# Optimization experiments

Hardware: AMD Instinct MI355X
Metric: run time of the kernel (lower is better)

Reference implementation:

```python
import jax, jax.numpy as jnp
import numpy as np

B, S, D, H = 2, 2048, 256, 8


def setup_inputs() -> dict:
    key = jax.random.key(0)
    ks = jax.random.split(key, 9)
    s = 1.0 / np.sqrt(D)
    x = jax.random.normal(ks[0], (B, S, D), dtype=jnp.float32)
    Wq = jax.random.normal(ks[1], (H, D, D), dtype=jnp.float32) * s
    Wk = jax.random.normal(ks[2], (H, D, D), dtype=jnp.float32) * s
    Wv = jax.random.normal(ks[3], (H, D, D), dtype=jnp.float32) * s
    bq = jnp.zeros((H, D), dtype=jnp.float32)
    bk = jnp.zeros((H, D), dtype=jnp.float32)
    bv = jnp.zeros((H, D), dtype=jnp.float32)
    Wo = jax.random.normal(ks[4], (H * D, D), dtype=jnp.float32) * (1.0 / np.sqrt(H * D))
    bo = jnp.zeros((D,), dtype=jnp.float32)
    return {"x": x, "Wq": Wq, "bq": bq, "Wk": Wk, "bk": bk, "Wv": Wv, "bv": bv, "Wo": Wo, "bo": bo}


def reference(x, Wq, bq, Wk, bk, Wv, bv, Wo, bo):
    # Per-head Q/K/V projections, batched over heads via einsum.
    # q,k,v: [B, H, S, D]
    q = jnp.einsum('bsd,hde->bhse', x, Wq) + bq[None, :, None, :]
    k = jnp.einsum('bsd,hde->bhse', x, Wk) + bk[None, :, None, :]
    v = jnp.einsum('bsd,hde->bhse', x, Wv) + bv[None, :, None, :]
    scale = 1.0 / jnp.sqrt(jnp.asarray(D, dtype=x.dtype))
    scores = jnp.einsum('bhse,bhte->bhst', q, k) * scale  # [B,H,S,S]
    attn = jax.nn.softmax(scores, axis=-1)
    o = jnp.einsum('bhst,bhte->bhse', attn, v)  # [B,H,S,D]
    # Concat heads along feature dim: [B,S,H*D]
    concat = o.transpose(0, 2, 1, 3).reshape(B, S, H * D)
    return concat @ Wo + bo
```

## Files before the change

### kernel.cpp

```cpp
#include <hip/hip_runtime.h>

typedef __bf16 bf16x8 __attribute__((ext_vector_type(8)));
typedef __bf16 bf16x4 __attribute__((ext_vector_type(4)));
typedef float  f32x4  __attribute__((ext_vector_type(4)));
typedef float  f32x16 __attribute__((ext_vector_type(16)));

#define DEVI __device__ __forceinline__

DEVI bf16x8 ld8(const __bf16* p) { return *reinterpret_cast<const bf16x8*>(p); }
DEVI f32x4 mfma16(bf16x8 a, bf16x8 b, f32x4 c) {
  return __builtin_amdgcn_mfma_f32_16x16x32_bf16(a, b, c, 0, 0, 0);
}
DEVI f32x16 mfma32(bf16x8 a, bf16x8 b, f32x16 c) {
  return __builtin_amdgcn_mfma_f32_32x32x16_bf16(a, b, c, 0, 0, 0);
}
DEVI void gl_lds16(const void* g, void* l) {
  __builtin_amdgcn_global_load_lds((__attribute__((address_space(1))) void*)g,
                                   (__attribute__((address_space(3))) void*)l, 16, 0, 0);
}
DEVI unsigned pk2(float a, float b) {
  union { __bf16 h[2]; unsigned u; } x;
  x.h[0] = (__bf16)a; x.h[1] = (__bf16)b; return x.u;
}

#if __has_builtin(__builtin_amdgcn_exp2f)
#define EXP2(x) __builtin_amdgcn_exp2f(x)
#else
#define EXP2(x) exp2f(x)
#endif

__global__ __launch_bounds__(256) void k_prep(
    const float* __restrict__ x, const float* __restrict__ Wq,
    const float* __restrict__ Wk, const float* __restrict__ Wv,
    const float* __restrict__ Wo, __bf16* __restrict__ xb,
    __bf16* __restrict__ Wt, __bf16* __restrict__ Woh, __bf16* __restrict__ Wol) {
  const int bid = blockIdx.x;
  if (bid < 1024) {
    const int i = bid * 256 + threadIdx.x;
    f32x4 v = reinterpret_cast<const f32x4*>(x)[i];
    bf16x4 o;
    o[0] = (__bf16)v[0]; o[1] = (__bf16)v[1]; o[2] = (__bf16)v[2]; o[3] = (__bf16)v[3];
    reinterpret_cast<bf16x4*>(xb)[i] = o;
    return;
  }
  __shared__ float t[32][33];
  const int flat = bid - 1024;
  const float* in; __bf16* oh; __bf16* ol = nullptr;
  int R, C, c0, r0;
  bool lo = false;
  if (flat < 1536) {
    const int which = flat >> 9, rem = flat & 511;
    const int h = rem >> 6, tt = rem & 63;
    c0 = (tt & 7) * 32; r0 = (tt >> 3) * 32;
    const float* Wsrc = which == 0 ? Wq : which == 1 ? Wk : Wv;
    in = Wsrc + h * 65536;
    oh = Wt + which * 524288 + h * 65536;
    R = 256; C = 256;
  } else {
    const int rem = flat - 1536;
    c0 = (rem & 7) * 32; r0 = (rem >> 3) * 32;
    in = Wo; oh = Woh; ol = Wol; lo = true;
    R = 2048; C = 256;
  }
  const int tx = threadIdx.x & 31, ty = threadIdx.x >> 5;
  #pragma unroll
  for (int k = 0; k < 32; k += 8)
    t[ty + k][tx] = in[(size_t)(r0 + ty + k) * C + c0 + tx];
  __syncthreads();
  #pragma unroll
  for (int k = 0; k < 32; k += 8) {
    const float v = t[tx][ty + k];
    const size_t o = (size_t)(c0 + ty + k) * R + r0 + tx;
    const __bf16 h = (__bf16)v;
    oh[o] = h;
    if (lo) ol[o] = (__bf16)(v - (float)h);
  }
}

__global__ __launch_bounds__(256) void k_qkv(
    const __bf16* __restrict__ xb, const __bf16* __restrict__ Wt,
    const float* __restrict__ bq, const float* __restrict__ bk, const float* __restrict__ bv,
    __bf16* __restrict__ Qb, __bf16* __restrict__ Kb, __bf16* __restrict__ Vtb) {
  const int wl = threadIdx.x >> 6, lane = threadIdx.x & 63;
  const int g = lane >> 4, qc = lane & 15;
  const int which = blockIdx.z >> 3, h = blockIdx.z & 7;
  const int sblk = blockIdx.x * 256;
  const int s0 = sblk + wl * 64;
  const int e0 = blockIdx.y * 64;
  const __bf16* Wm = Wt + ((size_t)blockIdx.z << 16);
  const float* bias = (which == 0 ? bq : which == 1 ? bk : bv) + h * 256;
  const int b = sblk >> 11;
  const int bh = b * 8 + h;
  const int sm0 = s0 & 2047;
  f32x4 acc[4][4] = {};

  if (which == 2) {
    #pragma unroll
    for (int kk = 0; kk < 8; kk++) {
      bf16x8 af[4], bf[4];
      #pragma unroll
      for (int ai = 0; ai < 4; ai++)
        af[ai] = ld8(xb + (size_t)(s0 + ai * 16 + qc) * 256 + kk * 32 + g * 8);
      #pragma unroll
      for (int bj = 0; bj < 4; bj++)
        bf[bj] = ld8(Wm + (size_t)(e0 + bj * 16 + qc) * 256 + kk * 32 + g * 8);
      #pragma unroll
      for (int ai = 0; ai < 4; ai++)
        #pragma unroll
        for (int bj = 0; bj < 4; bj++)
          acc[ai][bj] = mfma16(af[ai], bf[bj], acc[ai][bj]);
    }
    #pragma unroll
    for (int bj = 0; bj < 4; bj++) {
      const int e = e0 + bj * 16 + qc;
      const float be = bias[e];
      #pragma unroll
      for (int ai = 0; ai < 4; ai++) {
        bf16x4 pk;
        #pragma unroll
        for (int r = 0; r < 4; r++) pk[r] = (__bf16)(acc[ai][bj][r] + be);
        *reinterpret_cast<bf16x4*>(Vtb + ((size_t)(bh * 256 + e)) * 2048 +
                                   sm0 + ai * 16 + g * 4) = pk;
      }
    }
  } else {
    #pragma unroll
    for (int kk = 0; kk < 8; kk++) {
      bf16x8 af[4], bf[4];
      #pragma unroll
      for (int ai = 0; ai < 4; ai++)
        af[ai] = ld8(Wm + (size_t)(e0 + ai * 16 + qc) * 256 + kk * 32 + g * 8);
      #pragma unroll
      for (int bj = 0; bj < 4; bj++)
        bf[bj] = ld8(xb + (size_t)(s0 + bj * 16 + qc) * 256 + kk * 32 + g * 8);
      #pragma unroll
      for (int ai = 0; ai < 4; ai++)
        #pragma unroll
        for (int bj = 0; bj < 4; bj++)
          acc[ai][bj] = mfma16(af[ai], bf[bj], acc[ai][bj]);
    }
    const float sc = (which == 0) ? 0.0625f * 1.4426950408889634f : 1.0f;
    __bf16* Out = (which == 0) ? Qb : Kb;
    float be[4][4];
    #pragma unroll
    for (int ai = 0; ai < 4; ai++)
      #pragma unroll
      for (int r = 0; r < 4; r++) be[ai][r] = bias[e0 + ai * 16 + g * 4 + r];
    #pragma unroll
    for (int ai = 0; ai < 4; ai++)
      #pragma unroll
      for (int bj = 0; bj < 4; bj++) {
        const int srow = sm0 + bj * 16 + qc;
        bf16x4 pk;
        #pragma unroll
        for (int r = 0; r < 4; r++)
          pk[r] = (__bf16)((acc[ai][bj][r] + be[ai][r]) * sc);
        *reinterpret_cast<bf16x4*>(Out + ((size_t)(bh * 2048 + srow)) * 256 +
                                   e0 + ai * 16 + g * 4) = pk;
      }
  }
}

__global__ __launch_bounds__(256) void k_attn(
    const __bf16* __restrict__ Qb, const __bf16* __restrict__ Kb,
    const __bf16* __restrict__ Vtb, __bf16* __restrict__ Oh, __bf16* __restrict__ Ol) {
  __shared__ __align__(16) unsigned char smem[131072];
  const int tid = threadIdx.x;
  const int wl = tid >> 6, lane = tid & 63;
  const int hi = lane >> 5, q = lane & 31;

  const int bid = blockIdx.x;
  const int s = (bid & 7) * 32 + (bid >> 3);
  const int bh = s >> 4, qt = s & 15;

  const int q0w = qt * 128 + wl * 32;
  const char* Kg = (const char*)Kb + ((size_t)bh * 2048) * 512;
  const char* Vg = (const char*)Vtb + (size_t)bh * 256 * 4096;
  const __bf16* Qp = Qb + ((size_t)(bh * 2048 + q0w + q)) * 256;

  bf16x8 qf[16];
  #pragma unroll
  for (int kk = 0; kk < 16; kk++) qf[kk] = ld8(Qp + kk * 16 + hi * 8);

  f32x16 acc[8];
  #pragma unroll
  for (int i = 0; i < 8; i++)
    #pragma unroll
    for (int e = 0; e < 16; e++) acc[i][e] = 0.f;

  auto stage = [&](int nb, int t) {
    unsigned char* kbp = smem + nb * 32768 + wl * 8192;
    unsigned char* vbp = smem + 65536 + nb * 32768 + wl * 8192;
    #pragma unroll
    for (int j = 0; j < 8; j++) {
      const int O = wl * 8192 + j * 1024 + lane * 16;
      const int kv = O >> 9;
      const int c = ((O >> 4) & 31) ^ (kv & 15);
      gl_lds16(Kg + (size_t)t * 32768 + (size_t)kv * 512 + c * 16, kbp + j * 1024);
    }
    #pragma unroll
    for (int j = 0; j < 8; j++) {
      const int O = wl * 8192 + j * 1024 + lane * 16;
      const int sb = O >> 10;
      const int kvh = (O >> 9) & 1;
      const int dlo = (O >> 6) & 7;
      const int ci = (O >> 4) & 3;
      const int d = sb * 8 + dlo;
      gl_lds16(Vg + (size_t)d * 4096 + (size_t)t * 128 + kvh * 64 + ((ci ^ (sb & 3)) << 4),
               vbp + j * 1024);
    }
  };

  float m_run = -3.0e38f, l_run = 0.f;
  stage(0, 0);
  __syncthreads();

  for (int t = 0; t < 32; t++) {
    const int cur = t & 1;
    const unsigned char* kbc = smem + cur * 32768;
    const unsigned char* vbc = smem + 65536 + cur * 32768;
    if (t < 31) stage(cur ^ 1, t + 1);

    f32x16 st0, st1;
    #pragma unroll
    for (int e = 0; e < 16; e++) { st0[e] = 0.f; st1[e] = 0.f; }
    __builtin_amdgcn_s_setprio(1);
    #pragma unroll
    for (int kk = 0; kk < 16; kk++) {
      const int o0 = q * 512 + ((((kk << 1) + hi) ^ (q & 15)) << 4);
      bf16x8 k0 = *reinterpret_cast<const bf16x8*>(kbc + o0);
      bf16x8 k1 = *reinterpret_cast<const bf16x8*>(kbc + o0 + 16384);
      st0 = mfma32(k0, qf[kk], st0);
      st1 = mfma32(k1, qf[kk], st1);
    }
    __builtin_amdgcn_s_setprio(0);

    f32x16 mx;
    #pragma unroll
    for (int r = 0; r < 16; r++) mx[r] = fmaxf(st0[r], st1[r]);
    #pragma unroll
    for (int w2 = 8; w2 > 0; w2 >>= 1)
      #pragma unroll
      for (int r = 0; r < w2; r++) mx[r] = fmaxf(mx[r], mx[r + w2]);
    const float rmax = fmaxf(mx[0], __shfl_xor(mx[0], 32));
    if (__any(rmax > m_run + 8.0f)) {
      const float m_new = fmaxf(rmax, m_run);
      const float alpha = EXP2(m_run - m_new);
      m_run = m_new;
      l_run *= alpha;
      #pragma unroll
      for (int r = 0; r < 16; r++) {
        const float ar = __shfl(alpha, (r & 3) + 8 * (r >> 2) + 4 * hi);
        #pragma unroll
        for (int dt = 0; dt < 8; dt++) acc[dt][r] *= ar;
      }
    }
    f32x16 sm_;
    #pragma unroll
    for (int r = 0; r < 16; r++) {
      st0[r] = EXP2(st0[r] - m_run);
      st1[r] = EXP2(st1[r] - m_run);
      sm_[r] = st0[r] + st1[r];
    }
    #pragma unroll
    for (int w2 = 8; w2 > 0; w2 >>= 1)
      #pragma unroll
      for (int r = 0; r < w2; r++) sm_[r] += sm_[r + w2];
    l_run += sm_[0] + __shfl_xor(sm_[0], 32);

    bf16x8 pa[4];
    #define MKCHUNK(STV, H2, OUT) {                          \
      const unsigned L0 = pk2(STV[H2 * 8 + 0], STV[H2 * 8 + 1]);  \
      const unsigned L1 = pk2(STV[H2 * 8 + 2], STV[H2 * 8 + 3]);  \
      const unsigned H0 = pk2(STV[H2 * 8 + 4], STV[H2 * 8 + 5]);  \
      const unsigned H1 = pk2(STV[H2 * 8 + 6], STV[H2 * 8 + 7]);  \
      const unsigned xL0 = __shfl_xor(L0, 32), xL1 = __shfl_xor(L1, 32); \
      const unsigned xH0 = __shfl_xor(H0, 32), xH1 = __shfl_xor(H1, 32); \
      unsigned pw[4];                                        \
      pw[0] = hi ? xH0 : L0;  pw[1] = hi ? xH1 : L1;         \
      pw[2] = hi ? H0 : xL0;  pw[3] = hi ? H1 : xL1;         \
      OUT = *reinterpret_cast<bf16x8*>(pw); }
    MKCHUNK(st0, 0, pa[0]); MKCHUNK(st0, 1, pa[1]);
    MKCHUNK(st1, 0, pa[2]); MKCHUNK(st1, 1, pa[3]);
    #undef MKCHUNK

    __builtin_amdgcn_s_setprio(1);
    #pragma unroll
    for (int dt = 0; dt < 8; dt++) {
      const int d = dt * 32 + q;
      const int base = (d >> 3) * 1024 + (d & 7) * 64;
      const int key = (d >> 3) & 3;
      #pragma unroll
      for (int c = 0; c < 4; c++) {
        const int off = base + (c >> 1) * 512 +
                        (((((c & 1) << 1) | hi) ^ key) << 4);
        bf16x8 vf = *reinterpret_cast<const bf16x8*>(vbc + off);
        acc[dt] = mfma32(pa[c], vf, acc[dt]);
      }
    }
    __builtin_amdgcn_s_setprio(0);
    __syncthreads();
  }

  float linv[16];
  #pragma unroll
  for (int r = 0; r < 16; r++)
    linv[r] = 1.f / __shfl(l_run, (r & 3) + 8 * (r >> 2) + 4 * hi);
  const int b = bh >> 3, h = bh & 7;
  #pragma unroll
  for (int dt = 0; dt < 8; dt++) {
    #pragma unroll
    for (int r = 0; r < 16; r++) {
      const float v = acc[dt][r] * linv[r];
      const int qrow = (r & 3) + 8 * (r >> 2) + 4 * hi;
      const size_t off = (size_t)b * (2048 * 2048) +
                         (size_t)(q0w + qrow) * 2048 + h * 256 + dt * 32 + q;
      const __bf16 hv = (__bf16)v;
      Oh[off] = hv;
      Ol[off] = (__bf16)(v - (float)hv);
    }
  }
}

__global__ __launch_bounds__(256) void k_out(
    const __bf16* __restrict__ Oh, const __bf16* __restrict__ Ol,
    const __bf16* __restrict__ Wh, const __bf16* __restrict__ Wl,
    const float* __restrict__ bo, float* __restrict__ out) {
  const int w = threadIdx.x >> 6, lane = threadIdx.x & 63;
  const int g = lane >> 4, qc = lane & 15;
  const int m0 = blockIdx.x * 64 + w * 16, n0 = blockIdx.y * 64;
  const int k0 = blockIdx.z * 1024;
  f32x4 acc[4] = {};
  const __bf16* ah_p = Oh + (size_t)(m0 + qc) * 2048 + k0 + g * 8;
  const __bf16* al_p = Ol + (size_t)(m0 + qc) * 2048 + k0 + g * 8;
  for (int kk = 0; kk < 32; kk++) {
    bf16x8 ah = ld8(ah_p + kk * 32);
    bf16x8 al = ld8(al_p + kk * 32);
    #pragma unroll
    for (int nt = 0; nt < 4; nt++) {
      const size_t nrow = (size_t)(n0 + nt * 16 + qc) * 2048 + k0 + kk * 32 + g * 8;
      bf16x8 bh = ld8(Wh + nrow);
      bf16x8 bl = ld8(Wl + nrow);
      acc[nt] = mfma16(ah, bh, acc[nt]);
      acc[nt] = mfma16(al, bh, acc[nt]);
      acc[nt] = mfma16(ah, bl, acc[nt]);
    }
  }
  #pragma unroll
  for (int nt = 0; nt < 4; nt++) {
    const int n = n0 + nt * 16 + qc;
    const float bb = (blockIdx.z == 0) ? bo[n] : 0.f;
    #pragma unroll
    for (int r = 0; r < 4; r++)
      unsafeAtomicAdd(&out[(m0 + g * 4 + r) * 256 + n], acc[nt][r] + bb);
  }
}

extern "C" void kernel_launch(void* const* d_in, const int* in_sizes, int n_in,
                              void* d_out, int out_size, void* d_ws, size_t ws_size,
                              hipStream_t stream) {
  const float* x  = (const float*)d_in[0];
  const float* Wq = (const float*)d_in[1];
  const float* bq = (const float*)d_in[2];
  const float* Wk = (const float*)d_in[3];
  const float* bk = (const float*)d_in[4];
  const float* Wv = (const float*)d_in[5];
  const float* bv = (const float*)d_in[6];
  const float* Wo = (const float*)d_in[7];
  const float* bo = (const float*)d_in[8];
  char* p = (char*)d_ws;
  __bf16* xb  = (__bf16*)(p);
  __bf16* Wt  = (__bf16*)(p + (2ull  << 20));
  __bf16* Woh = (__bf16*)(p + (5ull  << 20));
  __bf16* Wol = (__bf16*)(p + (6ull  << 20));
  __bf16* Qb  = (__bf16*)(p + (7ull  << 20));
  __bf16* Kb  = (__bf16*)(p + (23ull << 20));
  __bf16* Vtb = (__bf16*)(p + (39ull << 20));
  __bf16* Ohb = (__bf16*)(p + (55ull << 20));
  __bf16* Olb = (__bf16*)(p + (71ull << 20));

  k_prep<<<dim3(3072), dim3(256), 0, stream>>>(x, Wq, Wk, Wv, Wo, xb, Wt, Woh, Wol);
  k_qkv<<<dim3(16, 4, 24), dim3(256), 0, stream>>>(xb, Wt, bq, bk, bv, Qb, Kb, Vtb);
  k_attn<<<dim3(256), dim3(256), 0, stream>>>(Qb, Kb, Vtb, Ohb, Olb);
  (void)hipMemsetAsync(d_out, 0, (size_t)out_size * sizeof(float), stream);
  k_out<<<dim3(64, 4, 2), dim3(256), 0, stream>>>(Ohb, Olb, Woh, Wol, bo, (float*)d_out);
}
```

Measured before the change: 255.4 us.

## Fuse Q and K projections per block, drop setprio, deepen out-proj split-K

The QKV kernel now computes Q and K together in one block, sharing the x fragment loads across both weight matrices, and runs V in separate blocks, which cuts the grid from 24 to 16 z-slices. The s_setprio hints around the MFMA loops in the attention kernel are removed. The output projection's split-K factor goes from 2 to 4, halving each block's K range and doubling the number of atomic partial sums into the output. The QK fusion doubles accumulator registers per thread, which may lower occupancy.

```diff
diff --git a/kernel.cpp b/kernel.cpp
--- a/kernel.cpp
+++ b/kernel.cpp
@@ -83,18 +83,18 @@
     __bf16* __restrict__ Qb, __bf16* __restrict__ Kb, __bf16* __restrict__ Vtb) {
   const int wl = threadIdx.x >> 6, lane = threadIdx.x & 63;
   const int g = lane >> 4, qc = lane & 15;
-  const int which = blockIdx.z >> 3, h = blockIdx.z & 7;
+  const int h = blockIdx.z >> 1, isV = blockIdx.z & 1;
   const int sblk = blockIdx.x * 256;
   const int s0 = sblk + wl * 64;
   const int e0 = blockIdx.y * 64;
-  const __bf16* Wm = Wt + ((size_t)blockIdx.z << 16);
-  const float* bias = (which == 0 ? bq : which == 1 ? bk : bv) + h * 256;
   const int b = sblk >> 11;
   const int bh = b * 8 + h;
   const int sm0 = s0 & 2047;
-  f32x4 acc[4][4] = {};
-
-  if (which == 2) {
+
+  if (isV) {
+    const __bf16* Wm = Wt + 2 * 524288 + (size_t)h * 65536;
+    const float* bias = bv + h * 256;
+    f32x4 acc[4][4] = {};
     #pragma unroll
     for (int kk = 0; kk < 8; kk++) {
       bf16x8 af[4], bf[4];
@@ -124,40 +124,51 @@
       }
     }
   } else {
+    const __bf16* WmQ = Wt + (size_t)h * 65536;
+    const __bf16* WmK = Wt + 524288 + (size_t)h * 65536;
+    f32x4 accq[4][4] = {}, acck[4][4] = {};
     #pragma unroll
     for (int kk = 0; kk < 8; kk++) {
-      bf16x8 af[4], bf[4];
-      #pragma unroll
-      for (int ai = 0; ai < 4; ai++)
-        af[ai] = ld8(Wm + (size_t)(e0 + ai * 16 + qc) * 256 + kk * 32 + g * 8);
+      bf16x8 aq[4], ak[4], bf[4];
+      #pragma unroll
+      for (int ai = 0; ai < 4; ai++) {
+        aq[ai] = ld8(WmQ + (size_t)(e0 + ai * 16 + qc) * 256 + kk * 32 + g * 8);
+        ak[ai] = ld8(WmK + (size_t)(e0 + ai * 16 + qc) * 256 + kk * 32 + g * 8);
+      }
       #pragma unroll
       for (int bj = 0; bj < 4; bj++)
         bf[bj] = ld8(xb + (size_t)(s0 + bj * 16 + qc) * 256 + kk * 32 + g * 8);
       #pragma unroll
       for (int ai = 0; ai < 4; ai++)
         #pragma unroll
-        for (int bj = 0; bj < 4; bj++)
-          acc[ai][bj] = mfma16(af[ai], bf[bj], acc[ai][bj]);
-    }
-    const float sc = (which == 0) ? 0.0625f * 1.4426950408889634f : 1.0f;
-    __bf16* Out = (which == 0) ? Qb : Kb;
-    float be[4][4];
-    #pragma unroll
-    for (int ai = 0; ai < 4; ai++)
-      #pragma unroll
-      for (int r = 0; r < 4; r++) be[ai][r] = bias[e0 + ai * 16 + g * 4 + r];
-    #pragma unroll
-    for (int ai = 0; ai < 4; ai++)
+        for (int bj = 0; bj < 4; bj++) {
+          accq[ai][bj] = mfma16(aq[ai], bf[bj], accq[ai][bj]);
+          acck[ai][bj] = mfma16(ak[ai], bf[bj], acck[ai][bj]);
+        }
+    }
+    const float sc = 0.0625f * 1.4426950408889634f;
+    #pragma unroll
+    for (int ai = 0; ai < 4; ai++) {
+      float beq[4], bek[4];
+      #pragma unroll
+      for (int r = 0; r < 4; r++) {
+        beq[r] = bq[h * 256 + e0 + ai * 16 + g * 4 + r];
+        bek[r] = bk[h * 256 + e0 + ai * 16 + g * 4 + r];
+      }
       #pragma unroll
       for (int bj = 0; bj < 4; bj++) {
         const int srow = sm0 + bj * 16 + qc;
-        bf16x4 pk;
-        #pragma unroll
-        for (int r = 0; r < 4; r++)
-          pk[r] = (__bf16)((acc[ai][bj][r] + be[ai][r]) * sc);
-        *reinterpret_cast<bf16x4*>(Out + ((size_t)(bh * 2048 + srow)) * 256 +
-                                   e0 + ai * 16 + g * 4) = pk;
-      }
+        const size_t base = ((size_t)(bh * 2048 + srow)) * 256 + e0 + ai * 16 + g * 4;
+        bf16x4 pq, pk;
+        #pragma unroll
+        for (int r = 0; r < 4; r++) {
+          pq[r] = (__bf16)((accq[ai][bj][r] + beq[r]) * sc);
+          pk[r] = (__bf16)(acck[ai][bj][r] + bek[r]);
+        }
+        *reinterpret_cast<bf16x4*>(Qb + base) = pq;
+        *reinterpret_cast<bf16x4*>(Kb + base) = pk;
+      }
+    }
   }
 }
 
@@ -224,7 +235,6 @@
     f32x16 st0, st1;
     #pragma unroll
     for (int e = 0; e < 16; e++) { st0[e] = 0.f; st1[e] = 0.f; }
-    __builtin_amdgcn_s_setprio(1);
     #pragma unroll
     for (int kk = 0; kk < 16; kk++) {
       const int o0 = q * 512 + ((((kk << 1) + hi) ^ (q & 15)) << 4);
@@ -233,7 +243,6 @@
       st0 = mfma32(k0, qf[kk], st0);
       st1 = mfma32(k1, qf[kk], st1);
     }
-    __builtin_amdgcn_s_setprio(0);
 
     f32x16 mx;
     #pragma unroll
@@ -284,7 +293,6 @@
     MKCHUNK(st1, 0, pa[2]); MKCHUNK(st1, 1, pa[3]);
     #undef MKCHUNK
 
-    __builtin_amdgcn_s_setprio(1);
     #pragma unroll
     for (int dt = 0; dt < 8; dt++) {
       const int d = dt * 32 + q;
@@ -298,7 +306,6 @@
         acc[dt] = mfma32(pa[c], vf, acc[dt]);
       }
     }
-    __builtin_amdgcn_s_setprio(0);
     __syncthreads();
   }
 
@@ -329,11 +336,11 @@
   const int w = threadIdx.x >> 6, lane = threadIdx.x & 63;
   const int g = lane >> 4, qc = lane & 15;
   const int m0 = blockIdx.x * 64 + w * 16, n0 = blockIdx.y * 64;
-  const int k0 = blockIdx.z * 1024;
+  const int k0 = blockIdx.z * 512;
   f32x4 acc[4] = {};
   const __bf16* ah_p = Oh + (size_t)(m0 + qc) * 2048 + k0 + g * 8;
   const __bf16* al_p = Ol + (size_t)(m0 + qc) * 2048 + k0 + g * 8;
-  for (int kk = 0; kk < 32; kk++) {
+  for (int kk = 0; kk < 16; kk++) {
     bf16x8 ah = ld8(ah_p + kk * 32);
     bf16x8 al = ld8(al_p + kk * 32);
     #pragma unroll
@@ -380,8 +387,8 @@
   __bf16* Olb = (__bf16*)(p + (71ull << 20));
 
   k_prep<<<dim3(3072), dim3(256), 0, stream>>>(x, Wq, Wk, Wv, Wo, xb, Wt, Woh, Wol);
-  k_qkv<<<dim3(16, 4, 24), dim3(256), 0, stream>>>(xb, Wt, bq, bk, bv, Qb, Kb, Vtb);
+  k_qkv<<<dim3(16, 4, 16), dim3(256), 0, stream>>>(xb, Wt, bq, bk, bv, Qb, Kb, Vtb);
   k_attn<<<dim3(256), dim3(256), 0, stream>>>(Qb, Kb, Vtb, Ohb, Olb);
   (void)hipMemsetAsync(d_out, 0, (size_t)out_size * sizeof(float), stream);
-  k_out<<<dim3(64, 4, 2), dim3(256), 0, stream>>>(Ohb, Olb, Woh, Wol, bo, (float*)d_out);
-}
+  k_out<<<dim3(64, 4, 4), dim3(256), 0, stream>>>(Ohb, Olb, Woh, Wol, bo, (float*)d_out);
+}
```

Result: no change. 251.4 us (median of 2 runs) (-1.5%).
